# Kernel tuning notes

Measured on AMD Instinct MI355X. Metric: run time of the kernel, lower is better.

## Reference

```python
import jax, jax.numpy as jnp
import numpy as np

B, S, D, H = 8, 1024, 1024, 16
DEPTH = D // H  # 64


def setup_inputs() -> dict:
    key = jax.random.key(0)
    ks = jax.random.split(key, 12)
    s = 1.0 / np.sqrt(D)
    return {
        "Q": jax.random.normal(ks[0], (B, S, D), jnp.float32),
        "K": jax.random.normal(ks[1], (B, S, D), jnp.float32),
        "V": jax.random.normal(ks[2], (B, S, D), jnp.float32),
        "mask": jnp.zeros((B, 1, 1, S), jnp.float32),
        "Wq": jax.random.normal(ks[3], (D, D), jnp.float32) * s,
        "bq": jnp.zeros((D,), jnp.float32),
        "Wk": jax.random.normal(ks[4], (D, D), jnp.float32) * s,
        "bk": jnp.zeros((D,), jnp.float32),
        "Wv": jax.random.normal(ks[5], (D, D), jnp.float32) * s,
        "bv": jnp.zeros((D,), jnp.float32),
        "Wo": jax.random.normal(ks[6], (D, D), jnp.float32) * s,
        "bo": jnp.zeros((D,), jnp.float32),
    }


def _split_heads(x):
    # [B,S,D] -> [B,H,S,depth]
    b, s, _ = x.shape
    return x.reshape(b, s, H, DEPTH).transpose(0, 2, 1, 3)


def reference(Q, K, V, mask, Wq, bq, Wk, bk, Wv, bv, Wo, bo):
    q = _split_heads(Q @ Wq + bq)  # [B,H,S,depth]
    k = _split_heads(K @ Wk + bk)
    v = _split_heads(V @ Wv + bv)
    scale = 1.0 / jnp.sqrt(jnp.asarray(DEPTH, q.dtype))
    scores = jnp.einsum('bhqd,bhkd->bhqk', q, k) * scale  # [B,H,Sq,Sk]
    scores = scores + mask * (-1e9)
    attn = jax.nn.softmax(scores, axis=-1)
    out = jnp.einsum('bhqk,bhkd->bhqd', attn, v)  # [B,H,S,depth]
    out = out.transpose(0, 2, 1, 3).reshape(Q.shape[0], Q.shape[1], D)
    out = out @ Wo + bo
    return out, attn
```

## Files before the change

### kernel.cpp

```cpp
#include <hip/hip_runtime.h>

#define Bb 8
#define Ss 1024
#define Dd 1024
#define Hh 16
#define DEPTHh 64
#define BSD (Bb*Ss*Dd)
#define DDn (Dd*Dd)

typedef __bf16 bf16x8 __attribute__((ext_vector_type(8)));
typedef float  f32x4  __attribute__((ext_vector_type(4)));

__device__ __forceinline__ unsigned short f2bf(float f){
  unsigned u = __float_as_uint(f);
  u = (u + 0x7fffu + ((u >> 16) & 1u)) >> 16;
  return (unsigned short)u;
}
__device__ __forceinline__ float bf2f(unsigned short h){
  return __uint_as_float(((unsigned)h) << 16);
}

__global__ __launch_bounds__(256) void cvt_bf16(const float4* __restrict__ in,
                                                ushort4* __restrict__ out, int n4){
  int i = blockIdx.x*256 + threadIdx.x;
  if (i >= n4) return;
  float4 v = in[i];
  ushort4 o; o.x = f2bf(v.x); o.y = f2bf(v.y); o.z = f2bf(v.z); o.w = f2bf(v.w);
  out[i] = o;
}

__global__ __launch_bounds__(256) void transpose_w(const float* __restrict__ W,
                                                   ushort* __restrict__ WT){
  __shared__ float tl[32][33];
  int tx = threadIdx.x, ty = threadIdx.y;
  int bx = blockIdx.x*32, by = blockIdx.y*32;
  #pragma unroll
  for (int i=0;i<32;i+=8) tl[ty+i][tx] = W[(by+ty+i)*Dd + bx+tx];
  __syncthreads();
  #pragma unroll
  for (int i=0;i<32;i+=8) WT[(bx+ty+i)*Dd + by+tx] = f2bf(tl[tx][ty+i]);
}

__global__ __launch_bounds__(512) void transpose_v(const ushort* __restrict__ vh,
                                                   ushort* __restrict__ vt){
  __shared__ ushort tl[64][65];
  int tx = threadIdx.x, ty = threadIdx.y;
  long base = (long)blockIdx.y * 65536;
  int s0 = blockIdx.x*64;
  #pragma unroll
  for (int i=0;i<64;i+=8) tl[ty+i][tx] = vh[base + (long)(s0+ty+i)*64 + tx];
  __syncthreads();
  #pragma unroll
  for (int i=0;i<64;i+=8) vt[base + (long)(ty+i)*1024 + s0 + tx] = tl[tx][ty+i];
}

enum { M_PROJ=0, M_SCORES=1, M_PV=2, M_FINAL=3 };

template<int MODE>
__global__ __launch_bounds__(256) void gemm_bt(
    const ushort* __restrict__ Aall, const ushort* __restrict__ Ball,
    int lda, int ldb, int K, long sA, long sB,
    float* __restrict__ outf, ushort* __restrict__ outh,
    const float* __restrict__ aux)
{
  __shared__ ushort As[64][40];
  __shared__ ushort Bs[64][40];
  const int z = blockIdx.z;
  const ushort* A  = Aall + (long)z*sA;
  const ushort* Bp = Ball + (long)z*sB;
  const int m0 = blockIdx.x*64, n0 = blockIdx.y*64;
  const int t = threadIdx.x;
  const int lane = t & 63, wave = t >> 6;
  const int wm = (wave>>1)*32, wn = (wave&1)*32;
  const int q = lane>>4, l16 = lane&15;
  const int srow = t>>2, scol = (t&3)*8;

  f32x4 acc[2][2] = {};

  for (int k0=0; k0<K; k0+=32){
    uint4 av = *(const uint4*)(A  + (long)(m0+srow)*lda + k0 + scol);
    uint4 bv = *(const uint4*)(Bp + (long)(n0+srow)*ldb + k0 + scol);
    __syncthreads();
    *(uint4*)(&As[srow][scol]) = av;
    *(uint4*)(&Bs[srow][scol]) = bv;
    __syncthreads();
    bf16x8 a0 = *(const bf16x8*)(&As[wm      + l16][q*8]);
    bf16x8 a1 = *(const bf16x8*)(&As[wm + 16 + l16][q*8]);
    bf16x8 b0 = *(const bf16x8*)(&Bs[wn      + l16][q*8]);
    bf16x8 b1 = *(const bf16x8*)(&Bs[wn + 16 + l16][q*8]);
    acc[0][0] = __builtin_amdgcn_mfma_f32_16x16x32_bf16(a0,b0,acc[0][0],0,0,0);
    acc[0][1] = __builtin_amdgcn_mfma_f32_16x16x32_bf16(a0,b1,acc[0][1],0,0,0);
    acc[1][0] = __builtin_amdgcn_mfma_f32_16x16x32_bf16(a1,b0,acc[1][0],0,0,0);
    acc[1][1] = __builtin_amdgcn_mfma_f32_16x16x32_bf16(a1,b1,acc[1][1],0,0,0);
  }

  #pragma unroll
  for (int ti=0; ti<2; ti++)
  #pragma unroll
  for (int tj=0; tj<2; tj++)
  #pragma unroll
  for (int r=0; r<4; r++){
    float v = acc[ti][tj][r];
    const int row = m0 + wm + ti*16 + q*4 + r;
    const int col = n0 + wn + tj*16 + l16;
    if (MODE == M_PROJ){
      v += aux[col];
      const int b = row>>10, s = row&1023, h = col>>6, d = col&63;
      outh[((long)((b*Hh + h)*Ss + s)<<6) + d] = f2bf(v);
    } else if (MODE == M_SCORES){
      const int b = z>>4;
      v = v*0.125f + aux[(b<<10) + col] * (-1e9f);
      outh[((long)z<<20) + ((long)row<<10) + col] = f2bf(v);
    } else if (MODE == M_PV){
      const int b = z>>4, h = z&15;
      outh[(((long)(b<<10) + row)<<10) + (h<<6) + col] = f2bf(v);
    } else {
      v += aux[col];
      outf[(long)row*Dd + col] = v;
    }
  }
}

__global__ __launch_bounds__(256) void softmax_rows(ushort* __restrict__ sc,
                                                    float* __restrict__ attn){
  const long row = (long)blockIdx.x*4 + (threadIdx.x>>6);
  const int lane = threadIdx.x & 63;
  ushort* srow = sc + (row<<10);
  const uint4* sv = (const uint4*)srow;
  uint4 c[2]; c[0] = sv[lane]; c[1] = sv[lane+64];
  float f[16];
  #pragma unroll
  for (int j=0;j<2;j++){
    const unsigned* wp = (const unsigned*)&c[j];
    #pragma unroll
    for (int i=0;i<4;i++){
      f[j*8+i*2]   = bf2f((unsigned short)(wp[i] & 0xffffu));
      f[j*8+i*2+1] = bf2f((unsigned short)(wp[i] >> 16));
    }
  }
  float m = -1e30f;
  #pragma unroll
  for (int i=0;i<16;i++) m = fmaxf(m, f[i]);
  #pragma unroll
  for (int off=32; off; off>>=1) m = fmaxf(m, __shfl_xor(m, off, 64));
  float ssum = 0.f;
  #pragma unroll
  for (int i=0;i<16;i++){ f[i] = __expf(f[i]-m); ssum += f[i]; }
  #pragma unroll
  for (int off=32; off; off>>=1) ssum += __shfl_xor(ssum, off, 64);
  const float inv = 1.0f / ssum;

  float4* arow = (float4*)(attn + (row<<10));
  #pragma unroll
  for (int j=0;j<2;j++){
    const int vidx = (j==0) ? lane : lane+64;
    float4 o0, o1;
    o0.x=f[j*8+0]*inv; o0.y=f[j*8+1]*inv; o0.z=f[j*8+2]*inv; o0.w=f[j*8+3]*inv;
    o1.x=f[j*8+4]*inv; o1.y=f[j*8+5]*inv; o1.z=f[j*8+6]*inv; o1.w=f[j*8+7]*inv;
    arow[vidx*2]   = o0;
    arow[vidx*2+1] = o1;
    unsigned w0 = (unsigned)f2bf(o0.x) | ((unsigned)f2bf(o0.y)<<16);
    unsigned w1 = (unsigned)f2bf(o0.z) | ((unsigned)f2bf(o0.w)<<16);
    unsigned w2 = (unsigned)f2bf(o1.x) | ((unsigned)f2bf(o1.y)<<16);
    unsigned w3 = (unsigned)f2bf(o1.z) | ((unsigned)f2bf(o1.w)<<16);
    uint4 ob; ob.x=w0; ob.y=w1; ob.z=w2; ob.w=w3;
    ((uint4*)srow)[vidx] = ob;
  }
}

extern "C" void kernel_launch(void* const* d_in, const int* in_sizes, int n_in,
                              void* d_out, int out_size, void* d_ws, size_t ws_size,
                              hipStream_t stream)
{
  (void)in_sizes; (void)n_in; (void)out_size; (void)ws_size;
  const float* Q    = (const float*)d_in[0];
  const float* Kin  = (const float*)d_in[1];
  const float* V    = (const float*)d_in[2];
  const float* mask = (const float*)d_in[3];
  const float* Wq   = (const float*)d_in[4];
  const float* bq   = (const float*)d_in[5];
  const float* Wk   = (const float*)d_in[6];
  const float* bk   = (const float*)d_in[7];
  const float* Wv   = (const float*)d_in[8];
  const float* bv   = (const float*)d_in[9];
  const float* Wo   = (const float*)d_in[10];
  const float* bo   = (const float*)d_in[11];
  float* out    = (float*)d_out;
  float* attn_f = out + (long)BSD;

  ushort* ws     = (ushort*)d_ws;
  ushort* Xq     = ws;
  ushort* Xk     = Xq  + (long)BSD;
  ushort* Xv     = Xk  + (long)BSD;
  ushort* WqT    = Xv  + (long)BSD;
  ushort* WkT    = WqT + (long)DDn;
  ushort* WvT    = WkT + (long)DDn;
  ushort* WoT    = WvT + (long)DDn;
  ushort* qh     = WoT + (long)DDn;
  ushort* kh     = qh  + (long)BSD;
  ushort* vt     = kh  + (long)BSD;
  ushort* attn_h = vt  + (long)BSD;
  ushort* vh     = attn_h;
  ushort* concat = Xq;

  cvt_bf16<<<dim3(BSD/4/256), 256, 0, stream>>>((const float4*)Q,   (ushort4*)Xq, BSD/4);
  cvt_bf16<<<dim3(BSD/4/256), 256, 0, stream>>>((const float4*)Kin, (ushort4*)Xk, BSD/4);
  cvt_bf16<<<dim3(BSD/4/256), 256, 0, stream>>>((const float4*)V,   (ushort4*)Xv, BSD/4);

  transpose_w<<<dim3(32,32), dim3(32,8), 0, stream>>>(Wq, WqT);
  transpose_w<<<dim3(32,32), dim3(32,8), 0, stream>>>(Wk, WkT);
  transpose_w<<<dim3(32,32), dim3(32,8), 0, stream>>>(Wv, WvT);
  transpose_w<<<dim3(32,32), dim3(32,8), 0, stream>>>(Wo, WoT);

  gemm_bt<M_PROJ><<<dim3(128,16,1), 256, 0, stream>>>(Xq, WqT, Dd, Dd, Dd, 0,0, nullptr, qh, bq);
  gemm_bt<M_PROJ><<<dim3(128,16,1), 256, 0, stream>>>(Xk, WkT, Dd, Dd, Dd, 0,0, nullptr, kh, bk);
  gemm_bt<M_PROJ><<<dim3(128,16,1), 256, 0, stream>>>(Xv, WvT, Dd, Dd, Dd, 0,0, nullptr, vh, bv);

  transpose_v<<<dim3(16,128), dim3(64,8), 0, stream>>>(vh, vt);

  gemm_bt<M_SCORES><<<dim3(16,16,128), 256, 0, stream>>>(qh, kh, 64, 64, 64,
                                                         65536, 65536, nullptr, attn_h, mask);

  softmax_rows<<<dim3(32768), 256, 0, stream>>>(attn_h, attn_f);

  gemm_bt<M_PV><<<dim3(16,1,128), 256, 0, stream>>>(attn_h, vt, 1024, 1024, 1024,
                                                    1048576, 65536, nullptr, concat, nullptr);

  gemm_bt<M_FINAL><<<dim3(128,16,1), 256, 0, stream>>>(concat, WoT, Dd, Dd, Dd,
                                                       0,0, out, nullptr, bo);
}
```

Measured before the change: 1.118 ms.

## Fuse scores, softmax and PV into a two-pass flash-style attention kernel

Replaces the separate scores GEMM, softmax and PV GEMM kernels with one fused kernel per (batch, head, 64-query tile). A first pass over the keys computes running row max and sum with an online softmax. A second pass recomputes the scores, writes the normalized fp32 attention probabilities, stages them as bf16 in LDS, and accumulates P·V directly. This removes the round trips of the bf16 score matrix through global memory, at the cost of computing QK^T twice. The fp32 attention stores are now scalar 64-byte segments rather than wide float4 stores.

```diff
diff --git a/kernel.cpp b/kernel.cpp
--- a/kernel.cpp
+++ b/kernel.cpp
@@ -54,7 +54,7 @@
   for (int i=0;i<64;i+=8) vt[base + (long)(ty+i)*1024 + s0 + tx] = tl[tx][ty+i];
 }
 
-enum { M_PROJ=0, M_SCORES=1, M_PV=2, M_FINAL=3 };
+enum { M_PROJ=0, M_FINAL=3 };
 
 template<int MODE>
 __global__ __launch_bounds__(256) void gemm_bt(
@@ -107,13 +107,6 @@
       v += aux[col];
       const int b = row>>10, s = row&1023, h = col>>6, d = col&63;
       outh[((long)((b*Hh + h)*Ss + s)<<6) + d] = f2bf(v);
-    } else if (MODE == M_SCORES){
-      const int b = z>>4;
-      v = v*0.125f + aux[(b<<10) + col] * (-1e9f);
-      outh[((long)z<<20) + ((long)row<<10) + col] = f2bf(v);
-    } else if (MODE == M_PV){
-      const int b = z>>4, h = z&15;
-      outh[(((long)(b<<10) + row)<<10) + (h<<6) + col] = f2bf(v);
     } else {
       v += aux[col];
       outf[(long)row*Dd + col] = v;
@@ -121,50 +114,191 @@
   }
 }
 
-__global__ __launch_bounds__(256) void softmax_rows(ushort* __restrict__ sc,
-                                                    float* __restrict__ attn){
-  const long row = (long)blockIdx.x*4 + (threadIdx.x>>6);
-  const int lane = threadIdx.x & 63;
-  ushort* srow = sc + (row<<10);
-  const uint4* sv = (const uint4*)srow;
-  uint4 c[2]; c[0] = sv[lane]; c[1] = sv[lane+64];
-  float f[16];
-  #pragma unroll
-  for (int j=0;j<2;j++){
-    const unsigned* wp = (const unsigned*)&c[j];
-    #pragma unroll
-    for (int i=0;i<4;i++){
-      f[j*8+i*2]   = bf2f((unsigned short)(wp[i] & 0xffffu));
-      f[j*8+i*2+1] = bf2f((unsigned short)(wp[i] >> 16));
-    }
-  }
-  float m = -1e30f;
-  #pragma unroll
-  for (int i=0;i<16;i++) m = fmaxf(m, f[i]);
-  #pragma unroll
-  for (int off=32; off; off>>=1) m = fmaxf(m, __shfl_xor(m, off, 64));
-  float ssum = 0.f;
-  #pragma unroll
-  for (int i=0;i<16;i++){ f[i] = __expf(f[i]-m); ssum += f[i]; }
-  #pragma unroll
-  for (int off=32; off; off>>=1) ssum += __shfl_xor(ssum, off, 64);
-  const float inv = 1.0f / ssum;
-
-  float4* arow = (float4*)(attn + (row<<10));
-  #pragma unroll
-  for (int j=0;j<2;j++){
-    const int vidx = (j==0) ? lane : lane+64;
-    float4 o0, o1;
-    o0.x=f[j*8+0]*inv; o0.y=f[j*8+1]*inv; o0.z=f[j*8+2]*inv; o0.w=f[j*8+3]*inv;
-    o1.x=f[j*8+4]*inv; o1.y=f[j*8+5]*inv; o1.z=f[j*8+6]*inv; o1.w=f[j*8+7]*inv;
-    arow[vidx*2]   = o0;
-    arow[vidx*2+1] = o1;
-    unsigned w0 = (unsigned)f2bf(o0.x) | ((unsigned)f2bf(o0.y)<<16);
-    unsigned w1 = (unsigned)f2bf(o0.z) | ((unsigned)f2bf(o0.w)<<16);
-    unsigned w2 = (unsigned)f2bf(o1.x) | ((unsigned)f2bf(o1.y)<<16);
-    unsigned w3 = (unsigned)f2bf(o1.z) | ((unsigned)f2bf(o1.w)<<16);
-    uint4 ob; ob.x=w0; ob.y=w1; ob.z=w2; ob.w=w3;
-    ((uint4*)srow)[vidx] = ob;
+__global__ __launch_bounds__(256) void attn_fused(
+    const ushort* __restrict__ qh,
+    const ushort* __restrict__ kh,
+    const ushort* __restrict__ vt,
+    const float*  __restrict__ mask,
+    float* __restrict__ attn_f,
+    ushort* __restrict__ concat)
+{
+  __shared__ __align__(16) ushort qs[64][72];
+  __shared__ __align__(16) ushort ks[64][72];
+  __shared__ __align__(16) ushort vs[64][72];
+  __shared__ __align__(16) ushort ps[64][72];
+  __shared__ float red_m[2][64];
+  __shared__ float red_l[2][64];
+
+  const int z = blockIdx.z;
+  const int b = z >> 4, h = z & 15;
+  const int t = threadIdx.x;
+  const int lane = t & 63, wave = t >> 6;
+  const int wm = (wave >> 1) * 32;
+  const int wc = wave & 1;
+  const int wn = wc * 32;
+  const int q = lane >> 4, l16 = lane & 15;
+  const int srow = t >> 2, sc = (t & 3) * 8;
+
+  const ushort* qz = qh + ((long)z << 16);
+  const ushort* kz = kh + ((long)z << 16);
+  const ushort* vz = vt + ((long)z << 16);
+  const int q0 = blockIdx.x * 64;
+
+  {
+    const ushort* src = qz + (long)(q0 + srow) * 64 + sc;
+    *(uint4*)(&qs[srow][sc])      = *(const uint4*)(src);
+    *(uint4*)(&qs[srow][sc + 32]) = *(const uint4*)(src + 32);
+  }
+
+  float m_ln[2][4], l_ln[2][4];
+  #pragma unroll
+  for (int ti=0; ti<2; ti++)
+  #pragma unroll
+  for (int r=0; r<4; r++){ m_ln[ti][r] = -1e30f; l_ln[ti][r] = 0.f; }
+
+  for (int s = 0; s < 16; ++s){
+    const int k0 = s * 64;
+    const ushort* ksrc = kz + (long)(k0 + srow) * 64 + sc;
+    uint4 kv0 = *(const uint4*)(ksrc);
+    uint4 kv1 = *(const uint4*)(ksrc + 32);
+    __syncthreads();
+    *(uint4*)(&ks[srow][sc])      = kv0;
+    *(uint4*)(&ks[srow][sc + 32]) = kv1;
+    __syncthreads();
+
+    f32x4 accs[2][2] = {};
+    #pragma unroll
+    for (int kk=0; kk<2; ++kk){
+      bf16x8 a0 = *(const bf16x8*)(&qs[wm      + l16][kk*32 + q*8]);
+      bf16x8 a1 = *(const bf16x8*)(&qs[wm + 16 + l16][kk*32 + q*8]);
+      bf16x8 b0 = *(const bf16x8*)(&ks[wn      + l16][kk*32 + q*8]);
+      bf16x8 b1 = *(const bf16x8*)(&ks[wn + 16 + l16][kk*32 + q*8]);
+      accs[0][0] = __builtin_amdgcn_mfma_f32_16x16x32_bf16(a0,b0,accs[0][0],0,0,0);
+      accs[0][1] = __builtin_amdgcn_mfma_f32_16x16x32_bf16(a0,b1,accs[0][1],0,0,0);
+      accs[1][0] = __builtin_amdgcn_mfma_f32_16x16x32_bf16(a1,b0,accs[1][0],0,0,0);
+      accs[1][1] = __builtin_amdgcn_mfma_f32_16x16x32_bf16(a1,b1,accs[1][1],0,0,0);
+    }
+    const float mk0 = mask[(b<<10) + k0 + wn + l16]      * (-1e9f);
+    const float mk1 = mask[(b<<10) + k0 + wn + 16 + l16] * (-1e9f);
+    #pragma unroll
+    for (int ti=0; ti<2; ti++)
+    #pragma unroll
+    for (int r=0; r<4; r++){
+      const float s0 = accs[ti][0][r]*0.125f + mk0;
+      const float s1 = accs[ti][1][r]*0.125f + mk1;
+      const float mn = fmaxf(m_ln[ti][r], fmaxf(s0, s1));
+      l_ln[ti][r] = l_ln[ti][r]*__expf(m_ln[ti][r]-mn)
+                  + __expf(s0-mn) + __expf(s1-mn);
+      m_ln[ti][r] = mn;
+    }
+  }
+
+  #pragma unroll
+  for (int ti=0; ti<2; ti++)
+  #pragma unroll
+  for (int r=0; r<4; r++){
+    float m = m_ln[ti][r], l = l_ln[ti][r];
+    #pragma unroll
+    for (int off=1; off<16; off<<=1){
+      float om = __shfl_xor(m, off, 64);
+      float ol = __shfl_xor(l, off, 64);
+      float mn = fmaxf(m, om);
+      l = l*__expf(m-mn) + ol*__expf(om-mn);
+      m = mn;
+    }
+    m_ln[ti][r] = m; l_ln[ti][r] = l;
+  }
+  if (l16 == 0){
+    #pragma unroll
+    for (int ti=0; ti<2; ti++)
+    #pragma unroll
+    for (int r=0; r<4; r++){
+      const int row = wm + ti*16 + q*4 + r;
+      red_m[wc][row] = m_ln[ti][r];
+      red_l[wc][row] = l_ln[ti][r];
+    }
+  }
+  __syncthreads();
+  float m_fin[2][4], li[2][4];
+  #pragma unroll
+  for (int ti=0; ti<2; ti++)
+  #pragma unroll
+  for (int r=0; r<4; r++){
+    const int row = wm + ti*16 + q*4 + r;
+    const float m0 = red_m[0][row], m1 = red_m[1][row];
+    const float l0 = red_l[0][row], l1 = red_l[1][row];
+    const float mt = fmaxf(m0, m1);
+    const float lt = l0*__expf(m0-mt) + l1*__expf(m1-mt);
+    m_fin[ti][r] = mt;
+    li[ti][r] = 1.0f / lt;
+  }
+
+  f32x4 accp[2][2] = {};
+  for (int s = 0; s < 16; ++s){
+    const int k0 = s * 64;
+    const ushort* ksrc = kz + (long)(k0 + srow) * 64 + sc;
+    const ushort* vsrc = vz + (long)srow * 1024 + k0 + sc;
+    uint4 kv0 = *(const uint4*)(ksrc);
+    uint4 kv1 = *(const uint4*)(ksrc + 32);
+    uint4 vv0 = *(const uint4*)(vsrc);
+    uint4 vv1 = *(const uint4*)(vsrc + 32);
+    __syncthreads();
+    *(uint4*)(&ks[srow][sc])      = kv0;
+    *(uint4*)(&ks[srow][sc + 32]) = kv1;
+    *(uint4*)(&vs[srow][sc])      = vv0;
+    *(uint4*)(&vs[srow][sc + 32]) = vv1;
+    __syncthreads();
+
+    f32x4 accs[2][2] = {};
+    #pragma unroll
+    for (int kk=0; kk<2; ++kk){
+      bf16x8 a0 = *(const bf16x8*)(&qs[wm      + l16][kk*32 + q*8]);
+      bf16x8 a1 = *(const bf16x8*)(&qs[wm + 16 + l16][kk*32 + q*8]);
+      bf16x8 b0 = *(const bf16x8*)(&ks[wn      + l16][kk*32 + q*8]);
+      bf16x8 b1 = *(const bf16x8*)(&ks[wn + 16 + l16][kk*32 + q*8]);
+      accs[0][0] = __builtin_amdgcn_mfma_f32_16x16x32_bf16(a0,b0,accs[0][0],0,0,0);
+      accs[0][1] = __builtin_amdgcn_mfma_f32_16x16x32_bf16(a0,b1,accs[0][1],0,0,0);
+      accs[1][0] = __builtin_amdgcn_mfma_f32_16x16x32_bf16(a1,b0,accs[1][0],0,0,0);
+      accs[1][1] = __builtin_amdgcn_mfma_f32_16x16x32_bf16(a1,b1,accs[1][1],0,0,0);
+    }
+    const float mk0 = mask[(b<<10) + k0 + wn + l16]      * (-1e9f);
+    const float mk1 = mask[(b<<10) + k0 + wn + 16 + l16] * (-1e9f);
+    #pragma unroll
+    for (int ti=0; ti<2; ti++)
+    #pragma unroll
+    for (int r=0; r<4; r++){
+      const int row = wm + ti*16 + q*4 + r;
+      const float p0 = __expf(accs[ti][0][r]*0.125f + mk0 - m_fin[ti][r]) * li[ti][r];
+      const float p1 = __expf(accs[ti][1][r]*0.125f + mk1 - m_fin[ti][r]) * li[ti][r];
+      float* arow = attn_f + (((long)z<<20) + ((long)(q0+row)<<10) + k0);
+      arow[wn + l16]      = p0;
+      arow[wn + 16 + l16] = p1;
+      ps[row][wn + l16]      = f2bf(p0);
+      ps[row][wn + 16 + l16] = f2bf(p1);
+    }
+    __syncthreads();
+    #pragma unroll
+    for (int kk=0; kk<2; ++kk){
+      bf16x8 a0 = *(const bf16x8*)(&ps[wm      + l16][kk*32 + q*8]);
+      bf16x8 a1 = *(const bf16x8*)(&ps[wm + 16 + l16][kk*32 + q*8]);
+      bf16x8 b0 = *(const bf16x8*)(&vs[wn      + l16][kk*32 + q*8]);
+      bf16x8 b1 = *(const bf16x8*)(&vs[wn + 16 + l16][kk*32 + q*8]);
+      accp[0][0] = __builtin_amdgcn_mfma_f32_16x16x32_bf16(a0,b0,accp[0][0],0,0,0);
+      accp[0][1] = __builtin_amdgcn_mfma_f32_16x16x32_bf16(a0,b1,accp[0][1],0,0,0);
+      accp[1][0] = __builtin_amdgcn_mfma_f32_16x16x32_bf16(a1,b0,accp[1][0],0,0,0);
+      accp[1][1] = __builtin_amdgcn_mfma_f32_16x16x32_bf16(a1,b1,accp[1][1],0,0,0);
+    }
+  }
+
+  #pragma unroll
+  for (int mi=0; mi<2; mi++)
+  #pragma unroll
+  for (int nj=0; nj<2; nj++)
+  #pragma unroll
+  for (int r=0; r<4; r++){
+    const int row = q0 + wm + mi*16 + q*4 + r;
+    const int d   = wn + nj*16 + l16;
+    concat[(((long)(b<<10) + row)<<10) + (h<<6) + d] = f2bf(accp[mi][nj][r]);
   }
 }
 
@@ -199,8 +333,7 @@
   ushort* qh     = WoT + (long)DDn;
   ushort* kh     = qh  + (long)BSD;
   ushort* vt     = kh  + (long)BSD;
-  ushort* attn_h = vt  + (long)BSD;
-  ushort* vh     = attn_h;
+  ushort* vh     = vt  + (long)BSD;
   ushort* concat = Xq;
 
   cvt_bf16<<<dim3(BSD/4/256), 256, 0, stream>>>((const float4*)Q,   (ushort4*)Xq, BSD/4);
@@ -218,13 +351,7 @@
 
   transpose_v<<<dim3(16,128), dim3(64,8), 0, stream>>>(vh, vt);
 
-  gemm_bt<M_SCORES><<<dim3(16,16,128), 256, 0, stream>>>(qh, kh, 64, 64, 64,
-                                                         65536, 65536, nullptr, attn_h, mask);
-
-  softmax_rows<<<dim3(32768), 256, 0, stream>>>(attn_h, attn_f);
-
-  gemm_bt<M_PV><<<dim3(16,1,128), 256, 0, stream>>>(attn_h, vt, 1024, 1024, 1024,
-                                                    1048576, 65536, nullptr, concat, nullptr);
+  attn_fused<<<dim3(16,1,128), 256, 0, stream>>>(qh, kh, vt, mask, attn_f, concat);
 
   gemm_bt<M_FINAL><<<dim3(128,16,1), 256, 0, stream>>>(concat, WoT, Dd, Dd, Dd,
                                                        0,0, out, nullptr, bo);
```

After: 955.7 us. 1.17x faster.
